# Performance work log

Hardware: AMD Instinct MI355X
Metric: run time of the kernel (lower is better)

The kernel has to match this reference:

```python
import jax, jax.numpy as jnp
import numpy as np

PRE = 4096      # NMS_PRE_MAXSIZE
POST = 512      # NMS_POST_MAXSIZE
THRESH = 0.7    # NMS_THRESH


def setup_inputs() -> dict:
    key = jax.random.key(0)
    k1, k2, k3, k4, k5 = jax.random.split(key, 5)
    B, N, C = 4, 32768, 3
    # realistic lidar-frame boxes: (x, y, z, dx, dy, dz, heading)
    xy = jax.random.uniform(k1, (B, N, 2)) * 140.0 - 70.0
    z = jax.random.uniform(k2, (B, N, 1)) * 3.0 - 2.0
    dims = jax.random.uniform(k3, (B, N, 3)) * 4.0 + 1.0
    heading = jax.random.uniform(k4, (B, N, 1)) * (2.0 * np.pi) - np.pi
    batch_box_preds = jnp.concatenate([xy, z, dims, heading], axis=-1)
    batch_cls_preds = jax.random.normal(k5, (B, N, C))
    return {"batch_cls_preds": batch_cls_preds, "batch_box_preds": batch_box_preds}


def _bev_iou(boxes):
    # boxes: (K, 7); axis-aligned BEV IoU over (x, y, dx, dy) -> (K, K)
    x, y, dx, dy = boxes[:, 0], boxes[:, 1], boxes[:, 3], boxes[:, 4]
    x1, x2 = x - dx * 0.5, x + dx * 0.5
    y1, y2 = y - dy * 0.5, y + dy * 0.5
    ix = jnp.clip(jnp.minimum(x2[:, None], x2[None, :]) - jnp.maximum(x1[:, None], x1[None, :]), 0.0)
    iy = jnp.clip(jnp.minimum(y2[:, None], y2[None, :]) - jnp.maximum(y1[:, None], y1[None, :]), 0.0)
    inter = ix * iy
    area = dx * dy
    union = area[:, None] + area[None, :] - inter
    return inter / jnp.maximum(union, 1e-6)


def _class_agnostic_nms(scores, boxes):
    # scores: (N,), boxes: (N, 7) -> selected idx (POST,), scores (POST,), valid (POST,)
    topk_scores, idx = jax.lax.top_k(scores, PRE)          # score-sorted candidates
    iou = _bev_iou(boxes[idx])                              # (PRE, PRE)
    ar = jnp.arange(PRE)
    def body(i, keep):  # greedy suppression in score order
        sup = keep[i] & (iou[i] > THRESH) & (ar > i)
        return keep & ~sup
    keep = jax.lax.fori_loop(0, PRE, body, jnp.ones((PRE,), bool))
    order = jnp.argsort(jnp.where(keep, ar, PRE))           # stable: kept first, score order
    sel = order[:POST]
    valid = keep[sel]
    return idx[sel], topk_scores[sel] * valid, valid


def reference(batch_cls_preds, batch_box_preds):
    # argmax scoring over classes (torch.max(cls_preds, dim=1))
    roi_scores_all = jnp.max(batch_cls_preds, axis=-1)      # (B, N)
    roi_labels_all = jnp.argmax(batch_cls_preds, axis=-1)   # (B, N)

    def per_item(scores, labels, boxes):
        sel, sel_scores, valid = _class_agnostic_nms(scores, boxes)
        rois = boxes[sel] * valid[:, None].astype(boxes.dtype)   # zero-padded buffer
        roi_labels = jnp.where(valid, labels[sel], 0) + 1        # +1 applied to whole buffer
        return rois, sel_scores, roi_labels

    rois, roi_scores, roi_labels = jax.vmap(per_item)(roi_scores_all, roi_labels_all, batch_box_preds)
    return rois, roi_scores, roi_labels
```

## Files before the change

### kernel.cpp

```cpp
#include <hip/hip_runtime.h>
#include <stdint.h>

typedef unsigned long long u64;

#define BB 4
#define NN 32768
#define CC 3
#define PRE 4096
#define RNK 768
#define POST 512
#define TH 0.7f
#define ROWS_A 768
#define RW (ROWS_A / 64)
#define CANDCAP 2048
#define RS_TILE 2048

__device__ __forceinline__ uint32_t f2u(float f) {
    uint32_t b = __float_as_uint(f);
    return (b & 0x80000000u) ? ~b : (b | 0x80000000u);
}
__device__ __forceinline__ float u2f(uint32_t u) {
    uint32_t b = (u & 0x80000000u) ? (u & 0x7FFFFFFFu) : ~u;
    return __uint_as_float(b);
}
__device__ __forceinline__ float score3(const float* p) {
    return fmaxf(fmaxf(p[0], p[1]), p[2]);
}

__global__ void k_hist(const float* __restrict__ cls,
                       uint32_t* __restrict__ hist_f, uint32_t* __restrict__ hist_c,
                       uint32_t* __restrict__ scal) {
    __shared__ uint32_t lc[256];
    lc[threadIdx.x] = 0;
    if (blockIdx.x == 0 && threadIdx.x < 16) scal[threadIdx.x] = 0;
    __syncthreads();
    int gid = blockIdx.x * blockDim.x + threadIdx.x;
    int b = gid >> 15;
    uint32_t p16 = f2u(score3(cls + (size_t)gid * CC)) >> 16;
    atomicAdd(&hist_f[((uint32_t)b << 16) + p16], 1u);
    atomicAdd(&lc[p16 >> 8], 1u);
    __syncthreads();
    uint32_t v = lc[threadIdx.x];
    if (v) atomicAdd(&hist_c[((uint32_t)b << 8) + threadIdx.x], v);
}

__global__ void __launch_bounds__(256) k_collect(const float* __restrict__ cls,
                                                 const uint32_t* __restrict__ hist_c,
                                                 const uint32_t* __restrict__ hist_f,
                                                 uint32_t* __restrict__ cnt,
                                                 uint32_t* __restrict__ ccnt,
                                                 u64* __restrict__ selk, u64* __restrict__ cand) {
    int tid = threadIdx.x;
    int gid = blockIdx.x * 256 + tid;
    int b = gid >> 15;
    __shared__ uint32_t pref[256];
    __shared__ uint32_t s_selc, s_remc, s_pb;

    uint32_t v = hist_c[((uint32_t)b << 8) + 255 - tid];
    pref[tid] = v;
    __syncthreads();
    for (int off = 1; off < 256; off <<= 1) {
        uint32_t x = (tid >= off) ? pref[tid - off] : 0;
        __syncthreads();
        pref[tid] += x;
        __syncthreads();
    }
    {
        uint32_t after = pref[tid], before = after - v;
        if (before < RNK && RNK <= after) { s_selc = 255 - tid; s_remc = RNK - before; }
    }
    __syncthreads();
    uint32_t selc = s_selc, remc = s_remc;
    uint32_t v2 = hist_f[((uint32_t)b << 16) + (selc << 8) + 255 - tid];
    __syncthreads();
    pref[tid] = v2;
    __syncthreads();
    for (int off = 1; off < 256; off <<= 1) {
        uint32_t x = (tid >= off) ? pref[tid - off] : 0;
        __syncthreads();
        pref[tid] += x;
        __syncthreads();
    }
    {
        uint32_t after = pref[tid], before = after - v2;
        if (before < remc && remc <= after) s_pb = (selc << 8) | (uint32_t)(255 - tid);
    }
    __syncthreads();
    uint32_t pb = s_pb;

    u64 k = ((u64)f2u(score3(cls + (size_t)gid * CC)) << 32)
          | (uint32_t)(~(uint32_t)(gid & (NN - 1)));
    uint32_t p16 = (uint32_t)(k >> 48);
    bool def = p16 > pb;
    u64 mask = __ballot(def);
    int lane = tid & 63;
    int wave = tid >> 6;
    __shared__ uint32_t wtot[4], wbase[4], blockbase;
    uint32_t rank = lane ? (uint32_t)__popcll(mask & ((~0ull) >> (64 - lane))) : 0u;
    if (lane == 0) wtot[wave] = (uint32_t)__popcll(mask);
    __syncthreads();
    if (tid == 0) {
        uint32_t t = 0;
        for (int w = 0; w < 4; ++w) { wbase[w] = t; t += wtot[w]; }
        blockbase = atomicAdd(&cnt[b], t);
    }
    __syncthreads();
    if (def) {
        selk[(size_t)b * RNK + blockbase + wbase[wave] + rank] = k;
    } else if (p16 == pb) {
        uint32_t pos = atomicAdd(&ccnt[b], 1u);
        if (pos < CANDCAP) cand[(size_t)b * CANDCAP + pos] = k;
    }
}

__global__ void __launch_bounds__(256) k_rankscatter(const u64* __restrict__ selk,
                                                     const u64* __restrict__ cand,
                                                     const uint32_t* __restrict__ cnt,
                                                     const uint32_t* __restrict__ ccnt,
                                                     const float* __restrict__ box,
                                                     int* __restrict__ sidx,
                                                     float* __restrict__ ssc,
                                                     float* __restrict__ bf) {
    const int bpi = RS_TILE / 64;
    int b = blockIdx.x / bpi;
    int c = blockIdx.x % bpi;
    uint32_t base = cnt[b];
    uint32_t cc = ccnt[b]; if (cc > CANDCAP) cc = CANDCAP;
    uint32_t m = base + cc; if (m > RS_TILE) m = RS_TILE;
    if ((uint32_t)(c * 64) >= m) return;
    __shared__ u64 tile[RS_TILE];
    uint32_t mp = (m + 7) & ~7u;
    for (uint32_t i = threadIdx.x; i < mp; i += 256)
        tile[i] = (i < base) ? selk[(size_t)b * RNK + i]
                : (i < m)    ? cand[(size_t)b * CANDCAP + (i - base)] : 0ull;
    __syncthreads();
    uint32_t k = c * 64 + (threadIdx.x >> 2);
    u64 myk = tile[(k < m) ? k : 0];
    int q = threadIdx.x & 3;
    const ulonglong2* t2 = (const ulonglong2*)tile;
    int cn = 0;
#pragma unroll 8
    for (uint32_t j = 0; j < mp / 8; ++j) {
        ulonglong2 w = t2[4 * j + q];
        cn += (w.x > myk) ? 1 : 0;
        cn += (w.y > myk) ? 1 : 0;
    }
    cn += __shfl_xor(cn, 1, 64);
    cn += __shfl_xor(cn, 2, 64);
    if (q == 0 && k < m && cn < RNK) {
        int r = cn;
        int n = (int)(~(uint32_t)(myk & 0xFFFFFFFFull));
        float sc = u2f((uint32_t)(myk >> 32));
        sidx[b * RNK + r] = n;
        ssc[b * RNK + r] = sc;
        const float* bp = box + ((size_t)b * NN + n) * 7;
        float x = bp[0], y = bp[1], dx = bp[3], dy = bp[4];
        float* bfb = bf + (size_t)b * 5 * RNK;
        bfb[0 * RNK + r] = x - dx * 0.5f;
        bfb[1 * RNK + r] = x + dx * 0.5f;
        bfb[2 * RNK + r] = y - dy * 0.5f;
        bfb[3 * RNK + r] = y + dy * 0.5f;
        bfb[4 * RNK + r] = dx * dy;
    }
}

__global__ void k_iou(const float* __restrict__ bf, u64* __restrict__ supt) {
    const int bpi = ROWS_A / 4;
    int b = blockIdx.x / bpi;
    int wave = threadIdx.x >> 6;
    int lane = threadIdx.x & 63;
    int i = (blockIdx.x % bpi) * 4 + wave;
    const float* bfb = bf + (size_t)b * 5 * RNK;
    float x1 = bfb[0 * RNK + i], x2 = bfb[1 * RNK + i];
    float y1 = bfb[2 * RNK + i], y2 = bfb[3 * RNK + i];
    float ar = bfb[4 * RNK + i];
    u64 myword = 0;
    for (int jw = 0; jw < RW; ++jw) {
        int j = jw * 64 + lane;
        float jx1 = bfb[0 * RNK + j], jx2 = bfb[1 * RNK + j];
        float jy1 = bfb[2 * RNK + j], jy2 = bfb[3 * RNK + j];
        float jar = bfb[4 * RNK + j];
        float ix = fminf(x2, jx2) - fmaxf(x1, jx1);
        ix = fmaxf(ix, 0.0f);
        float iy = fminf(y2, jy2) - fmaxf(y1, jy1);
        iy = fmaxf(iy, 0.0f);
        float inter = __fmul_rn(ix, iy);
        float uni = (ar + jar) - inter;
        float iou = inter / fmaxf(uni, 1e-6f);
        u64 bal = __ballot((iou > TH) && (j > i));
        if (jw == lane) myword = bal;
    }
    if (lane < RW) supt[((size_t)b * RW + lane) * ROWS_A + i] = myword;
}

__global__ void __launch_bounds__(512) k_nmsout(const u64* __restrict__ supt,
                                                const uint32_t* __restrict__ cnt,
                                                const uint32_t* __restrict__ ccnt,
                                                const int* __restrict__ sidx,
                                                const float* __restrict__ ssc,
                                                const float* __restrict__ box,
                                                const float* __restrict__ cls,
                                                float* __restrict__ out,
                                                uint32_t* __restrict__ okf) {
    int b = blockIdx.x;
    int tid = threadIdx.x;
    __shared__ u64 keepw[RW], nremw[RW];
    __shared__ uint32_t wpre[RW + 1];
    __shared__ int s_changed, s_done;
    const u64* sb = supt + (size_t)b * RW * ROWS_A;

    if (tid < RW) keepw[tid] = ~0ull;
    if (tid == 0) s_done = 0;
    __syncthreads();
    for (int it = 0; it < 48; ++it) {
        if (tid < RW) nremw[tid] = 0;
        if (tid == 0) s_changed = 0;
        __syncthreads();
        for (int tau = tid; tau < ROWS_A; tau += 512) {
            int w = tau >> 6;
            int r0 = (tau & 63) * 12;
            const u64* wp = sb + (size_t)w * ROWS_A;
            u64 acc = 0;
#pragma unroll
            for (int rr = 0; rr < 12; ++rr) {
                int r = r0 + rr;
                if ((keepw[r >> 6] >> (r & 63)) & 1ull) acc |= wp[r];
            }
            if (acc) atomicOr(&nremw[w], acc);
        }
        __syncthreads();
        if (tid < RW) {
            u64 nk = ~nremw[tid];
            if (nk != keepw[tid]) { s_changed = 1; keepw[tid] = nk; }
        }
        __syncthreads();
        if (!s_changed) { if (tid == 0) s_done = 1; break; }
    }
    __syncthreads();

    if (tid == 0) {
        uint32_t c = 0;
        for (int w = 0; w < RW; ++w) { wpre[w] = c; c += (uint32_t)__popcll(keepw[w]); }
        wpre[RW] = c;
        uint32_t cc = ccnt[b];
        bool tileok = (cnt[b] + cc) <= RS_TILE;
        int ok = (s_done && c >= POST && tileok) ? 1 : 0;
        okf[b] = (uint32_t)ok;
        s_changed = ok;
    }
    __syncthreads();
    if (!s_changed) return;

    for (int r = tid; r < ROWS_A; r += 512) {
        int w = r >> 6, bit = r & 63;
        u64 word = keepw[w];
        if (!((word >> bit) & 1ull)) continue;
        u64 mask = bit ? ((1ull << bit) - 1ull) : 0ull;
        uint32_t d = wpre[w] + (uint32_t)__popcll(word & mask);
        if (d < POST) {
            float* ro = out + ((size_t)b * POST + d) * 7;
            int n = sidx[b * RNK + r];
            const float* bp = box + ((size_t)b * NN + n) * 7;
#pragma unroll
            for (int t = 0; t < 7; ++t) ro[t] = bp[t];
            out[(size_t)BB * POST * 7 + b * POST + d] = ssc[b * RNK + r];
            const float* cp = cls + ((size_t)b * NN + n) * CC;
            float c0 = cp[0], c1 = cp[1], c2 = cp[2];
            int lbl = 0; float bst = c0;
            if (c1 > bst) { bst = c1; lbl = 1; }
            if (c2 > bst) { lbl = 2; }
            out[(size_t)BB * POST * 8 + b * POST + d] = (float)(lbl + 1);
        }
    }
}

__global__ void __launch_bounds__(1024) k_fallback(const uint32_t* __restrict__ okf,
                                                   const float* __restrict__ cls,
                                                   const float* __restrict__ box,
                                                   u64* __restrict__ fkey,
                                                   u64* __restrict__ fselk,
                                                   u64* __restrict__ fkr,
                                                   float* __restrict__ fbf,
                                                   float* __restrict__ out) {
    int b = blockIdx.x;
    if (okf[b]) return;
    int tid = threadIdx.x;
    size_t bo = (size_t)b * NN;

    for (int n = tid; n < NN; n += 1024)
        fkey[bo + n] = ((u64)f2u(score3(cls + (bo + n) * CC)) << 32)
                     | (uint32_t)(~(uint32_t)n);
    __syncthreads();

    __shared__ uint32_t hist[256];
    __shared__ u64 s_prefix;
    __shared__ uint32_t s_k;
    if (tid == 0) { s_prefix = 0; s_k = PRE; }
    __syncthreads();
    for (int pass = 0; pass < 8; ++pass) {
        if (tid < 256) hist[tid] = 0;
        __syncthreads();
        u64 prefix = s_prefix;
        int hi = 8 * pass;
        for (int i = tid; i < NN; i += 1024) {
            u64 k = fkey[bo + i];
            bool match = (pass == 0) || ((k >> (64 - hi)) == prefix);
            if (match) atomicAdd(&hist[(uint32_t)((k >> (56 - hi)) & 255u)], 1u);
        }
        __syncthreads();
        if (tid == 0) {
            uint32_t kneed = s_k, cum = 0; int chosen = 0;
            for (int d = 255; d >= 0; --d) {
                if (kneed <= cum + hist[d]) { chosen = d; break; }
                cum += hist[d];
            }
            s_k = kneed - cum;
            s_prefix = (prefix << 8) | (u64)(uint32_t)chosen;
        }
        __syncthreads();
    }
    u64 kstar = s_prefix;

    __shared__ uint32_t s_cnt;
    if (tid == 0) s_cnt = 0;
    __syncthreads();
    for (int i = tid; i < NN; i += 1024) {
        u64 k = fkey[bo + i];
        if (k >= kstar) {
            uint32_t pos = atomicAdd(&s_cnt, 1u);
            if (pos < PRE) fselk[(size_t)b * PRE + pos] = k;
        }
    }
    __syncthreads();

    __shared__ u64 tile[1024];
    u64 myk0 = fselk[(size_t)b * PRE + tid];
    u64 myk1 = fselk[(size_t)b * PRE + tid + 1024];
    u64 myk2 = fselk[(size_t)b * PRE + tid + 2048];
    u64 myk3 = fselk[(size_t)b * PRE + tid + 3072];
    int rc0 = 0, rc1 = 0, rc2 = 0, rc3 = 0;
    for (int t0 = 0; t0 < PRE; t0 += 1024) {
        tile[tid] = fselk[(size_t)b * PRE + t0 + tid];
        __syncthreads();
#pragma unroll 8
        for (int j = 0; j < 1024; ++j) {
            u64 t = tile[j];
            rc0 += (t > myk0) ? 1 : 0;
            rc1 += (t > myk1) ? 1 : 0;
            rc2 += (t > myk2) ? 1 : 0;
            rc3 += (t > myk3) ? 1 : 0;
        }
        __syncthreads();
    }
    {
        u64 ks[4] = {myk0, myk1, myk2, myk3};
        int rs[4] = {rc0, rc1, rc2, rc3};
#pragma unroll
        for (int j = 0; j < 4; ++j) {
            u64 k = ks[j]; int r = rs[j];
            fkr[(size_t)b * PRE + r] = k;
            int n = (int)(~(uint32_t)(k & 0xFFFFFFFFull));
            const float* bp = box + ((size_t)b * NN + n) * 7;
            float x = bp[0], y = bp[1], dx = bp[3], dy = bp[4];
            float* fb = fbf + (size_t)b * 5 * PRE;
            fb[0 * PRE + r] = x - dx * 0.5f;
            fb[1 * PRE + r] = x + dx * 0.5f;
            fb[2 * PRE + r] = y - dy * 0.5f;
            fb[3 * PRE + r] = y + dy * 0.5f;
            fb[4 * PRE + r] = dx * dy;
        }
    }
    __syncthreads();

    __shared__ u64 km[64];
    __shared__ uint32_t wpre[65];
    const float* fb = fbf + (size_t)b * 5 * PRE;
    if (tid < 64) km[tid] = ~0ull;
    __syncthreads();
    for (int i = 0; i < PRE - 1; ++i) {
        if ((km[i >> 6] >> (i & 63)) & 1ull) {
            float x1 = fb[0 * PRE + i], x2 = fb[1 * PRE + i];
            float y1 = fb[2 * PRE + i], y2 = fb[3 * PRE + i];
            float ar = fb[4 * PRE + i];
            for (int j = i + 1 + tid; j < PRE; j += 1024) {
                float ix = fminf(x2, fb[1 * PRE + j]) - fmaxf(x1, fb[0 * PRE + j]);
                ix = fmaxf(ix, 0.0f);
                float iy = fminf(y2, fb[3 * PRE + j]) - fmaxf(y1, fb[2 * PRE + j]);
                iy = fmaxf(iy, 0.0f);
                float inter = __fmul_rn(ix, iy);
                float uni = (ar + fb[4 * PRE + j]) - inter;
                float iou = inter / fmaxf(uni, 1e-6f);
                if (iou > TH) atomicAnd(&km[j >> 6], ~(1ull << (j & 63)));
            }
        }
        __syncthreads();
    }

    if (tid == 0) {
        uint32_t c = 0;
        for (int w = 0; w < 64; ++w) { wpre[w] = c; c += (uint32_t)__popcll(km[w]); }
        wpre[64] = c;
    }
    __syncthreads();
    uint32_t nkeep = wpre[64];
    for (int r = tid; r < PRE; r += 1024) {
        int w = r >> 6, bit = r & 63;
        u64 word = km[w];
        bool kept = (word >> bit) & 1ull;
        u64 mask = bit ? ((1ull << bit) - 1ull) : 0ull;
        uint32_t before = wpre[w] + (uint32_t)__popcll(word & mask);
        uint32_t d = kept ? before : (nkeep + (uint32_t)r - before);
        if (d < POST) {
            float* ro = out + ((size_t)b * POST + d) * 7;
            float* so = out + (size_t)BB * POST * 7 + b * POST + d;
            float* lo = out + (size_t)BB * POST * 8 + b * POST + d;
            if (kept) {
                u64 k = fkr[(size_t)b * PRE + r];
                int n = (int)(~(uint32_t)(k & 0xFFFFFFFFull));
                const float* bp = box + ((size_t)b * NN + n) * 7;
#pragma unroll
                for (int t = 0; t < 7; ++t) ro[t] = bp[t];
                *so = u2f((uint32_t)(k >> 32));
                const float* cp = cls + ((size_t)b * NN + n) * CC;
                float c0 = cp[0], c1 = cp[1], c2 = cp[2];
                int lbl = 0; float bst = c0;
                if (c1 > bst) { bst = c1; lbl = 1; }
                if (c2 > bst) { lbl = 2; }
                *lo = (float)(lbl + 1);
            } else {
#pragma unroll
                for (int t = 0; t < 7; ++t) ro[t] = 0.0f;
                *so = 0.0f;
                *lo = 1.0f;
            }
        }
    }
}

extern "C" void kernel_launch(void* const* d_in, const int* in_sizes, int n_in,
                              void* d_out, int out_size, void* d_ws, size_t ws_size,
                              hipStream_t stream) {
    const float* cls = (const float*)d_in[0];
    const float* box = (const float*)d_in[1];
    float* out = (float*)d_out;

    char* ws = (char*)d_ws;
    const size_t KB = 1024, MB = 1024 * 1024;
    size_t OFF_SUPT  = 0;
    size_t OFF_HISTF = 512 * KB;
    size_t OFF_HISTC = 1536 * KB;
    size_t OFF_CAND  = 1540 * KB;
    size_t OFF_SELK  = 1604 * KB;
    size_t OFF_BF    = 1664 * KB;
    size_t OFF_SIDX  = 1728 * KB;
    size_t OFF_SSC   = 1740 * KB;
    size_t OFF_SCAL  = 1752 * KB;
    size_t OFF_FKEY  = 2 * MB;
    size_t OFF_FSELK = 3 * MB;
    size_t OFF_FKR   = 3 * MB + 128 * KB;
    size_t OFF_FBF   = 3 * MB + 256 * KB;

    u64*      supt   = (u64*)(ws + OFF_SUPT);
    uint32_t* hist_f = (uint32_t*)(ws + OFF_HISTF);
    uint32_t* hist_c = (uint32_t*)(ws + OFF_HISTC);
    u64*      cand   = (u64*)(ws + OFF_CAND);
    u64*      selk   = (u64*)(ws + OFF_SELK);
    float*    bf     = (float*)(ws + OFF_BF);
    int*      sidx   = (int*)(ws + OFF_SIDX);
    float*    ssc    = (float*)(ws + OFF_SSC);
    uint32_t* scal   = (uint32_t*)(ws + OFF_SCAL);
    uint32_t* cnt    = scal;
    uint32_t* ccnt   = scal + 4;
    uint32_t* okf    = scal + 8;
    u64*      fkey   = (u64*)(ws + OFF_FKEY);
    u64*      fselk  = (u64*)(ws + OFF_FSELK);
    u64*      fkr    = (u64*)(ws + OFF_FKR);
    float*    fbf    = (float*)(ws + OFF_FBF);

    hipMemsetAsync(ws + OFF_HISTF, 0, MB + 4 * KB, stream);
    k_hist<<<(BB * NN) / 256, 256, 0, stream>>>(cls, hist_f, hist_c, scal);
    k_collect<<<(BB * NN) / 256, 256, 0, stream>>>(cls, hist_c, hist_f, cnt, ccnt, selk, cand);
    k_rankscatter<<<BB * (RS_TILE / 64), 256, 0, stream>>>(selk, cand, cnt, ccnt,
                                                           box, sidx, ssc, bf);
    k_iou<<<(ROWS_A / 4) * BB, 256, 0, stream>>>(bf, supt);
    k_nmsout<<<BB, 512, 0, stream>>>(supt, cnt, ccnt, sidx, ssc, box, cls, out, okf);
    k_fallback<<<BB, 1024, 0, stream>>>(okf, cls, box, fkey, fselk, fkr, fbf, out);
}
```

Baseline: 67.41 us.

## Vectorize hist/collect to 4 scores per thread and merge fallback into NMS kernel

```diff
diff --git a/kernel.cpp b/kernel.cpp
--- a/kernel.cpp
+++ b/kernel.cpp
@@ -34,14 +34,26 @@
     lc[threadIdx.x] = 0;
     if (blockIdx.x == 0 && threadIdx.x < 16) scal[threadIdx.x] = 0;
     __syncthreads();
-    int gid = blockIdx.x * blockDim.x + threadIdx.x;
-    int b = gid >> 15;
-    uint32_t p16 = f2u(score3(cls + (size_t)gid * CC)) >> 16;
-    atomicAdd(&hist_f[((uint32_t)b << 16) + p16], 1u);
-    atomicAdd(&lc[p16 >> 8], 1u);
-    __syncthreads();
-    uint32_t v = lc[threadIdx.x];
-    if (v) atomicAdd(&hist_c[((uint32_t)b << 8) + threadIdx.x], v);
+    int g = blockIdx.x * 256 + threadIdx.x;
+    int b = g >> 13;
+    const float4* p4 = (const float4*)(cls + (size_t)g * 12);
+    float4 a = p4[0], v = p4[1], c = p4[2];
+    uint32_t p0 = f2u(fmaxf(fmaxf(a.x, a.y), a.z)) >> 16;
+    uint32_t p1 = f2u(fmaxf(fmaxf(a.w, v.x), v.y)) >> 16;
+    uint32_t p2 = f2u(fmaxf(fmaxf(v.z, v.w), c.x)) >> 16;
+    uint32_t p3 = f2u(fmaxf(fmaxf(c.y, c.z), c.w)) >> 16;
+    uint32_t bo = (uint32_t)b << 16;
+    atomicAdd(&hist_f[bo + p0], 1u);
+    atomicAdd(&hist_f[bo + p1], 1u);
+    atomicAdd(&hist_f[bo + p2], 1u);
+    atomicAdd(&hist_f[bo + p3], 1u);
+    atomicAdd(&lc[p0 >> 8], 1u);
+    atomicAdd(&lc[p1 >> 8], 1u);
+    atomicAdd(&lc[p2 >> 8], 1u);
+    atomicAdd(&lc[p3 >> 8], 1u);
+    __syncthreads();
+    uint32_t cv = lc[threadIdx.x];
+    if (cv) atomicAdd(&hist_c[((uint32_t)b << 8) + threadIdx.x], cv);
 }
 
 __global__ void __launch_bounds__(256) k_collect(const float* __restrict__ cls,
@@ -51,8 +63,8 @@
                                                  uint32_t* __restrict__ ccnt,
                                                  u64* __restrict__ selk, u64* __restrict__ cand) {
     int tid = threadIdx.x;
-    int gid = blockIdx.x * 256 + tid;
-    int b = gid >> 15;
+    int g = blockIdx.x * 256 + tid;
+    int b = g >> 13;
     __shared__ uint32_t pref[256];
     __shared__ uint32_t s_selc, s_remc, s_pb;
 
@@ -88,28 +100,29 @@
     __syncthreads();
     uint32_t pb = s_pb;
 
-    u64 k = ((u64)f2u(score3(cls + (size_t)gid * CC)) << 32)
-          | (uint32_t)(~(uint32_t)(gid & (NN - 1)));
-    uint32_t p16 = (uint32_t)(k >> 48);
-    bool def = p16 > pb;
-    u64 mask = __ballot(def);
+    const float4* p4 = (const float4*)(cls + (size_t)g * 12);
+    float4 a = p4[0], vv = p4[1], c = p4[2];
+    float sc[4] = {fmaxf(fmaxf(a.x, a.y), a.z), fmaxf(fmaxf(a.w, vv.x), vv.y),
+                   fmaxf(fmaxf(vv.z, vv.w), c.x), fmaxf(fmaxf(c.y, c.z), c.w)};
     int lane = tid & 63;
-    int wave = tid >> 6;
-    __shared__ uint32_t wtot[4], wbase[4], blockbase;
-    uint32_t rank = lane ? (uint32_t)__popcll(mask & ((~0ull) >> (64 - lane))) : 0u;
-    if (lane == 0) wtot[wave] = (uint32_t)__popcll(mask);
-    __syncthreads();
-    if (tid == 0) {
-        uint32_t t = 0;
-        for (int w = 0; w < 4; ++w) { wbase[w] = t; t += wtot[w]; }
-        blockbase = atomicAdd(&cnt[b], t);
-    }
-    __syncthreads();
-    if (def) {
-        selk[(size_t)b * RNK + blockbase + wbase[wave] + rank] = k;
-    } else if (p16 == pb) {
-        uint32_t pos = atomicAdd(&ccnt[b], 1u);
-        if (pos < CANDCAP) cand[(size_t)b * CANDCAP + pos] = k;
+#pragma unroll
+    for (int e = 0; e < 4; ++e) {
+        int el = g * 4 + e;
+        u64 k = ((u64)f2u(sc[e]) << 32) | (uint32_t)(~(uint32_t)(el & (NN - 1)));
+        uint32_t p16 = (uint32_t)(k >> 48);
+        bool def = p16 > pb;
+        u64 mask = __ballot(def);
+        if (def) {
+            uint32_t rank = (uint32_t)__popcll(mask & ((1ull << lane) - 1ull));
+            int leader = (int)(__ffsll((long long)mask) - 1);
+            uint32_t base = 0;
+            if (lane == leader) base = atomicAdd(&cnt[b], (uint32_t)__popcll(mask));
+            base = (uint32_t)__shfl((int)base, leader, 64);
+            selk[(size_t)b * RNK + base + rank] = k;
+        } else if (p16 == pb) {
+            uint32_t pos = atomicAdd(&ccnt[b], 1u);
+            if (pos < CANDCAP) cand[(size_t)b * CANDCAP + pos] = k;
+        }
     }
 }
 
@@ -150,9 +163,8 @@
     if (q == 0 && k < m && cn < RNK) {
         int r = cn;
         int n = (int)(~(uint32_t)(myk & 0xFFFFFFFFull));
-        float sc = u2f((uint32_t)(myk >> 32));
         sidx[b * RNK + r] = n;
-        ssc[b * RNK + r] = sc;
+        ssc[b * RNK + r] = u2f((uint32_t)(myk >> 32));
         const float* bp = box + ((size_t)b * NN + n) * 7;
         float x = bp[0], y = bp[1], dx = bp[3], dy = bp[4];
         float* bfb = bf + (size_t)b * 5 * RNK;
@@ -177,15 +189,12 @@
     u64 myword = 0;
     for (int jw = 0; jw < RW; ++jw) {
         int j = jw * 64 + lane;
-        float jx1 = bfb[0 * RNK + j], jx2 = bfb[1 * RNK + j];
-        float jy1 = bfb[2 * RNK + j], jy2 = bfb[3 * RNK + j];
-        float jar = bfb[4 * RNK + j];
-        float ix = fminf(x2, jx2) - fmaxf(x1, jx1);
+        float ix = fminf(x2, bfb[1 * RNK + j]) - fmaxf(x1, bfb[0 * RNK + j]);
         ix = fmaxf(ix, 0.0f);
-        float iy = fminf(y2, jy2) - fmaxf(y1, jy1);
+        float iy = fminf(y2, bfb[3 * RNK + j]) - fmaxf(y1, bfb[2 * RNK + j]);
         iy = fmaxf(iy, 0.0f);
         float inter = __fmul_rn(ix, iy);
-        float uni = (ar + jar) - inter;
+        float uni = (ar + bfb[4 * RNK + j]) - inter;
         float iou = inter / fmaxf(uni, 1e-6f);
         u64 bal = __ballot((iou > TH) && (j > i));
         if (jw == lane) myword = bal;
@@ -193,19 +202,23 @@
     if (lane < RW) supt[((size_t)b * RW + lane) * ROWS_A + i] = myword;
 }
 
-__global__ void __launch_bounds__(512) k_nmsout(const u64* __restrict__ supt,
-                                                const uint32_t* __restrict__ cnt,
-                                                const uint32_t* __restrict__ ccnt,
-                                                const int* __restrict__ sidx,
-                                                const float* __restrict__ ssc,
-                                                const float* __restrict__ box,
-                                                const float* __restrict__ cls,
-                                                float* __restrict__ out,
-                                                uint32_t* __restrict__ okf) {
+__global__ void __launch_bounds__(1024) k_nmsout(const u64* __restrict__ supt,
+                                                 const uint32_t* __restrict__ cnt,
+                                                 const uint32_t* __restrict__ ccnt,
+                                                 const int* __restrict__ sidx,
+                                                 const float* __restrict__ ssc,
+                                                 const float* __restrict__ box,
+                                                 const float* __restrict__ cls,
+                                                 const float* __restrict__ bf,
+                                                 u64* __restrict__ fkey,
+                                                 u64* __restrict__ fselk,
+                                                 u64* __restrict__ fkr,
+                                                 float* __restrict__ fbf,
+                                                 float* __restrict__ out) {
     int b = blockIdx.x;
     int tid = threadIdx.x;
     __shared__ u64 keepw[RW], nremw[RW];
-    __shared__ uint32_t wpre[RW + 1];
+    __shared__ uint32_t wpre[65];
     __shared__ int s_changed, s_done;
     const u64* sb = supt + (size_t)b * RW * ROWS_A;
 
@@ -216,7 +229,7 @@
         if (tid < RW) nremw[tid] = 0;
         if (tid == 0) s_changed = 0;
         __syncthreads();
-        for (int tau = tid; tau < ROWS_A; tau += 512) {
+        for (int tau = tid; tau < ROWS_A; tau += 1024) {
             int w = tau >> 6;
             int r0 = (tau & 63) * 12;
             const u64* wp = sb + (size_t)w * ROWS_A;
@@ -242,51 +255,37 @@
         uint32_t c = 0;
         for (int w = 0; w < RW; ++w) { wpre[w] = c; c += (uint32_t)__popcll(keepw[w]); }
         wpre[RW] = c;
-        uint32_t cc = ccnt[b];
-        bool tileok = (cnt[b] + cc) <= RS_TILE;
-        int ok = (s_done && c >= POST && tileok) ? 1 : 0;
-        okf[b] = (uint32_t)ok;
-        s_changed = ok;
-    }
-    __syncthreads();
-    if (!s_changed) return;
-
-    for (int r = tid; r < ROWS_A; r += 512) {
-        int w = r >> 6, bit = r & 63;
-        u64 word = keepw[w];
-        if (!((word >> bit) & 1ull)) continue;
-        u64 mask = bit ? ((1ull << bit) - 1ull) : 0ull;
-        uint32_t d = wpre[w] + (uint32_t)__popcll(word & mask);
-        if (d < POST) {
-            float* ro = out + ((size_t)b * POST + d) * 7;
-            int n = sidx[b * RNK + r];
-            const float* bp = box + ((size_t)b * NN + n) * 7;
-#pragma unroll
-            for (int t = 0; t < 7; ++t) ro[t] = bp[t];
-            out[(size_t)BB * POST * 7 + b * POST + d] = ssc[b * RNK + r];
-            const float* cp = cls + ((size_t)b * NN + n) * CC;
-            float c0 = cp[0], c1 = cp[1], c2 = cp[2];
-            int lbl = 0; float bst = c0;
-            if (c1 > bst) { bst = c1; lbl = 1; }
-            if (c2 > bst) { lbl = 2; }
-            out[(size_t)BB * POST * 8 + b * POST + d] = (float)(lbl + 1);
-        }
-    }
-}
-
-__global__ void __launch_bounds__(1024) k_fallback(const uint32_t* __restrict__ okf,
-                                                   const float* __restrict__ cls,
-                                                   const float* __restrict__ box,
-                                                   u64* __restrict__ fkey,
-                                                   u64* __restrict__ fselk,
-                                                   u64* __restrict__ fkr,
-                                                   float* __restrict__ fbf,
-                                                   float* __restrict__ out) {
-    int b = blockIdx.x;
-    if (okf[b]) return;
-    int tid = threadIdx.x;
+        bool tileok = (cnt[b] + ccnt[b]) <= RS_TILE;
+        s_changed = (s_done && c >= POST && tileok) ? 1 : 0;
+    }
+    __syncthreads();
+
+    if (s_changed) {
+        for (int r = tid; r < ROWS_A; r += 1024) {
+            int w = r >> 6, bit = r & 63;
+            u64 word = keepw[w];
+            if (!((word >> bit) & 1ull)) continue;
+            u64 mask = bit ? ((1ull << bit) - 1ull) : 0ull;
+            uint32_t d = wpre[w] + (uint32_t)__popcll(word & mask);
+            if (d < POST) {
+                float* ro = out + ((size_t)b * POST + d) * 7;
+                int n = sidx[b * RNK + r];
+                const float* bp = box + ((size_t)b * NN + n) * 7;
+#pragma unroll
+                for (int t = 0; t < 7; ++t) ro[t] = bp[t];
+                out[(size_t)BB * POST * 7 + b * POST + d] = ssc[b * RNK + r];
+                const float* cp = cls + ((size_t)b * NN + n) * CC;
+                float c0 = cp[0], c1 = cp[1], c2 = cp[2];
+                int lbl = 0; float bst = c0;
+                if (c1 > bst) { bst = c1; lbl = 1; }
+                if (c2 > bst) { lbl = 2; }
+                out[(size_t)BB * POST * 8 + b * POST + d] = (float)(lbl + 1);
+            }
+        }
+        return;
+    }
+
     size_t bo = (size_t)b * NN;
-
     for (int n = tid; n < NN; n += 1024)
         fkey[bo + n] = ((u64)f2u(score3(cls + (bo + n) * CC)) << 32)
                      | (uint32_t)(~(uint32_t)n);
@@ -373,7 +372,6 @@
     __syncthreads();
 
     __shared__ u64 km[64];
-    __shared__ uint32_t wpre[65];
     const float* fb = fbf + (size_t)b * 5 * PRE;
     if (tid < 64) km[tid] = ~0ull;
     __syncthreads();
@@ -471,18 +469,17 @@
     uint32_t* scal   = (uint32_t*)(ws + OFF_SCAL);
     uint32_t* cnt    = scal;
     uint32_t* ccnt   = scal + 4;
-    uint32_t* okf    = scal + 8;
     u64*      fkey   = (u64*)(ws + OFF_FKEY);
     u64*      fselk  = (u64*)(ws + OFF_FSELK);
     u64*      fkr    = (u64*)(ws + OFF_FKR);
     float*    fbf    = (float*)(ws + OFF_FBF);
 
     hipMemsetAsync(ws + OFF_HISTF, 0, MB + 4 * KB, stream);
-    k_hist<<<(BB * NN) / 256, 256, 0, stream>>>(cls, hist_f, hist_c, scal);
-    k_collect<<<(BB * NN) / 256, 256, 0, stream>>>(cls, hist_c, hist_f, cnt, ccnt, selk, cand);
+    k_hist<<<128, 256, 0, stream>>>(cls, hist_f, hist_c, scal);
+    k_collect<<<128, 256, 0, stream>>>(cls, hist_c, hist_f, cnt, ccnt, selk, cand);
     k_rankscatter<<<BB * (RS_TILE / 64), 256, 0, stream>>>(selk, cand, cnt, ccnt,
                                                            box, sidx, ssc, bf);
     k_iou<<<(ROWS_A / 4) * BB, 256, 0, stream>>>(bf, supt);
-    k_nmsout<<<BB, 512, 0, stream>>>(supt, cnt, ccnt, sidx, ssc, box, cls, out, okf);
-    k_fallback<<<BB, 1024, 0, stream>>>(okf, cls, box, fkey, fselk, fkr, fbf, out);
-}
+    k_nmsout<<<BB, 1024, 0, stream>>>(supt, cnt, ccnt, sidx, ssc, box, cls, bf,
+                                      fkey, fselk, fkr, fbf, out);
+}
```

Result: slower. 70.97 us (+5.3%).

## Merge fallback into NMS output kernel and replace memset with zero kernel

Applied to the files above, without the earlier changes.

```diff
diff --git a/kernel.cpp b/kernel.cpp
--- a/kernel.cpp
+++ b/kernel.cpp
@@ -27,12 +27,16 @@
     return fmaxf(fmaxf(p[0], p[1]), p[2]);
 }
 
+__global__ void k_zero(uint4* __restrict__ histreg, uint32_t* __restrict__ scal, int n16) {
+    int gid = blockIdx.x * blockDim.x + threadIdx.x;
+    if (gid < n16) histreg[gid] = make_uint4(0, 0, 0, 0);
+    if (gid < 16) scal[gid] = 0;
+}
+
 __global__ void k_hist(const float* __restrict__ cls,
-                       uint32_t* __restrict__ hist_f, uint32_t* __restrict__ hist_c,
-                       uint32_t* __restrict__ scal) {
+                       uint32_t* __restrict__ hist_f, uint32_t* __restrict__ hist_c) {
     __shared__ uint32_t lc[256];
     lc[threadIdx.x] = 0;
-    if (blockIdx.x == 0 && threadIdx.x < 16) scal[threadIdx.x] = 0;
     __syncthreads();
     int gid = blockIdx.x * blockDim.x + threadIdx.x;
     int b = gid >> 15;
@@ -150,9 +154,8 @@
     if (q == 0 && k < m && cn < RNK) {
         int r = cn;
         int n = (int)(~(uint32_t)(myk & 0xFFFFFFFFull));
-        float sc = u2f((uint32_t)(myk >> 32));
         sidx[b * RNK + r] = n;
-        ssc[b * RNK + r] = sc;
+        ssc[b * RNK + r] = u2f((uint32_t)(myk >> 32));
         const float* bp = box + ((size_t)b * NN + n) * 7;
         float x = bp[0], y = bp[1], dx = bp[3], dy = bp[4];
         float* bfb = bf + (size_t)b * 5 * RNK;
@@ -177,15 +180,12 @@
     u64 myword = 0;
     for (int jw = 0; jw < RW; ++jw) {
         int j = jw * 64 + lane;
-        float jx1 = bfb[0 * RNK + j], jx2 = bfb[1 * RNK + j];
-        float jy1 = bfb[2 * RNK + j], jy2 = bfb[3 * RNK + j];
-        float jar = bfb[4 * RNK + j];
-        float ix = fminf(x2, jx2) - fmaxf(x1, jx1);
+        float ix = fminf(x2, bfb[1 * RNK + j]) - fmaxf(x1, bfb[0 * RNK + j]);
         ix = fmaxf(ix, 0.0f);
-        float iy = fminf(y2, jy2) - fmaxf(y1, jy1);
+        float iy = fminf(y2, bfb[3 * RNK + j]) - fmaxf(y1, bfb[2 * RNK + j]);
         iy = fmaxf(iy, 0.0f);
         float inter = __fmul_rn(ix, iy);
-        float uni = (ar + jar) - inter;
+        float uni = (ar + bfb[4 * RNK + j]) - inter;
         float iou = inter / fmaxf(uni, 1e-6f);
         u64 bal = __ballot((iou > TH) && (j > i));
         if (jw == lane) myword = bal;
@@ -193,19 +193,22 @@
     if (lane < RW) supt[((size_t)b * RW + lane) * ROWS_A + i] = myword;
 }
 
-__global__ void __launch_bounds__(512) k_nmsout(const u64* __restrict__ supt,
-                                                const uint32_t* __restrict__ cnt,
-                                                const uint32_t* __restrict__ ccnt,
-                                                const int* __restrict__ sidx,
-                                                const float* __restrict__ ssc,
-                                                const float* __restrict__ box,
-                                                const float* __restrict__ cls,
-                                                float* __restrict__ out,
-                                                uint32_t* __restrict__ okf) {
+__global__ void __launch_bounds__(1024) k_nmsout(const u64* __restrict__ supt,
+                                                 const uint32_t* __restrict__ cnt,
+                                                 const uint32_t* __restrict__ ccnt,
+                                                 const int* __restrict__ sidx,
+                                                 const float* __restrict__ ssc,
+                                                 const float* __restrict__ box,
+                                                 const float* __restrict__ cls,
+                                                 u64* __restrict__ fkey,
+                                                 u64* __restrict__ fselk,
+                                                 u64* __restrict__ fkr,
+                                                 float* __restrict__ fbf,
+                                                 float* __restrict__ out) {
     int b = blockIdx.x;
     int tid = threadIdx.x;
     __shared__ u64 keepw[RW], nremw[RW];
-    __shared__ uint32_t wpre[RW + 1];
+    __shared__ uint32_t wpre[65];
     __shared__ int s_changed, s_done;
     const u64* sb = supt + (size_t)b * RW * ROWS_A;
 
@@ -216,7 +219,7 @@
         if (tid < RW) nremw[tid] = 0;
         if (tid == 0) s_changed = 0;
         __syncthreads();
-        for (int tau = tid; tau < ROWS_A; tau += 512) {
+        for (int tau = tid; tau < ROWS_A; tau += 1024) {
             int w = tau >> 6;
             int r0 = (tau & 63) * 12;
             const u64* wp = sb + (size_t)w * ROWS_A;
@@ -242,51 +245,37 @@
         uint32_t c = 0;
         for (int w = 0; w < RW; ++w) { wpre[w] = c; c += (uint32_t)__popcll(keepw[w]); }
         wpre[RW] = c;
-        uint32_t cc = ccnt[b];
-        bool tileok = (cnt[b] + cc) <= RS_TILE;
-        int ok = (s_done && c >= POST && tileok) ? 1 : 0;
-        okf[b] = (uint32_t)ok;
-        s_changed = ok;
-    }
-    __syncthreads();
-    if (!s_changed) return;
-
-    for (int r = tid; r < ROWS_A; r += 512) {
-        int w = r >> 6, bit = r & 63;
-        u64 word = keepw[w];
-        if (!((word >> bit) & 1ull)) continue;
-        u64 mask = bit ? ((1ull << bit) - 1ull) : 0ull;
-        uint32_t d = wpre[w] + (uint32_t)__popcll(word & mask);
-        if (d < POST) {
-            float* ro = out + ((size_t)b * POST + d) * 7;
-            int n = sidx[b * RNK + r];
-            const float* bp = box + ((size_t)b * NN + n) * 7;
+        bool tileok = (cnt[b] + ccnt[b]) <= RS_TILE;
+        s_changed = (s_done && c >= POST && tileok) ? 1 : 0;
+    }
+    __syncthreads();
+
+    if (s_changed) {
+        for (int r = tid; r < ROWS_A; r += 1024) {
+            int w = r >> 6, bit = r & 63;
+            u64 word = keepw[w];
+            if (!((word >> bit) & 1ull)) continue;
+            u64 mask = bit ? ((1ull << bit) - 1ull) : 0ull;
+            uint32_t d = wpre[w] + (uint32_t)__popcll(word & mask);
+            if (d < POST) {
+                float* ro = out + ((size_t)b * POST + d) * 7;
+                int n = sidx[b * RNK + r];
+                const float* bp = box + ((size_t)b * NN + n) * 7;
 #pragma unroll
-            for (int t = 0; t < 7; ++t) ro[t] = bp[t];
-            out[(size_t)BB * POST * 7 + b * POST + d] = ssc[b * RNK + r];
-            const float* cp = cls + ((size_t)b * NN + n) * CC;
-            float c0 = cp[0], c1 = cp[1], c2 = cp[2];
-            int lbl = 0; float bst = c0;
-            if (c1 > bst) { bst = c1; lbl = 1; }
-            if (c2 > bst) { lbl = 2; }
-            out[(size_t)BB * POST * 8 + b * POST + d] = (float)(lbl + 1);
-        }
-    }
-}
-
-__global__ void __launch_bounds__(1024) k_fallback(const uint32_t* __restrict__ okf,
-                                                   const float* __restrict__ cls,
-                                                   const float* __restrict__ box,
-                                                   u64* __restrict__ fkey,
-                                                   u64* __restrict__ fselk,
-                                                   u64* __restrict__ fkr,
-                                                   float* __restrict__ fbf,
-                                                   float* __restrict__ out) {
-    int b = blockIdx.x;
-    if (okf[b]) return;
-    int tid = threadIdx.x;
+                for (int t = 0; t < 7; ++t) ro[t] = bp[t];
+                out[(size_t)BB * POST * 7 + b * POST + d] = ssc[b * RNK + r];
+                const float* cp = cls + ((size_t)b * NN + n) * CC;
+                float c0 = cp[0], c1 = cp[1], c2 = cp[2];
+                int lbl = 0; float bst = c0;
+                if (c1 > bst) { bst = c1; lbl = 1; }
+                if (c2 > bst) { lbl = 2; }
+                out[(size_t)BB * POST * 8 + b * POST + d] = (float)(lbl + 1);
+            }
+        }
+        return;
+    }
+
     size_t bo = (size_t)b * NN;
-
     for (int n = tid; n < NN; n += 1024)
         fkey[bo + n] = ((u64)f2u(score3(cls + (bo + n) * CC)) << 32)
                      | (uint32_t)(~(uint32_t)n);
@@ -373,7 +362,6 @@
     __syncthreads();
 
     __shared__ u64 km[64];
-    __shared__ uint32_t wpre[65];
     const float* fb = fbf + (size_t)b * 5 * PRE;
     if (tid < 64) km[tid] = ~0ull;
     __syncthreads();
@@ -471,18 +459,18 @@
     uint32_t* scal   = (uint32_t*)(ws + OFF_SCAL);
     uint32_t* cnt    = scal;
     uint32_t* ccnt   = scal + 4;
-    uint32_t* okf    = scal + 8;
     u64*      fkey   = (u64*)(ws + OFF_FKEY);
     u64*      fselk  = (u64*)(ws + OFF_FSELK);
     u64*      fkr    = (u64*)(ws + OFF_FKR);
     float*    fbf    = (float*)(ws + OFF_FBF);
 
-    hipMemsetAsync(ws + OFF_HISTF, 0, MB + 4 * KB, stream);
-    k_hist<<<(BB * NN) / 256, 256, 0, stream>>>(cls, hist_f, hist_c, scal);
+    int n16 = (int)((MB + 4 * KB) / 16);
+    k_zero<<<(n16 + 255) / 256, 256, 0, stream>>>((uint4*)(ws + OFF_HISTF), scal, n16);
+    k_hist<<<(BB * NN) / 256, 256, 0, stream>>>(cls, hist_f, hist_c);
     k_collect<<<(BB * NN) / 256, 256, 0, stream>>>(cls, hist_c, hist_f, cnt, ccnt, selk, cand);
     k_rankscatter<<<BB * (RS_TILE / 64), 256, 0, stream>>>(selk, cand, cnt, ccnt,
                                                            box, sidx, ssc, bf);
     k_iou<<<(ROWS_A / 4) * BB, 256, 0, stream>>>(bf, supt);
-    k_nmsout<<<BB, 512, 0, stream>>>(supt, cnt, ccnt, sidx, ssc, box, cls, out, okf);
-    k_fallback<<<BB, 1024, 0, stream>>>(okf, cls, box, fkey, fselk, fkr, fbf, out);
-}
+    k_nmsout<<<BB, 1024, 0, stream>>>(supt, cnt, ccnt, sidx, ssc, box, cls,
+                                      fkey, fselk, fkr, fbf, out);
+}
```

Result: faster. 64.93 us (median of 2 runs) (-3.7%).
